# Kernel tuning notes

Hardware: AMD Instinct MI355X
Metric: run time of the kernel (lower is better)

The kernel has to match this reference:

```python
import jax, jax.numpy as jnp
import numpy as np

B, N, C = 512, 252, 256  # N == C - 4 (class axis for torch-style CE over dim 1)


def setup_inputs() -> dict:
    key = jax.random.key(0)
    k1, k2, k3, k4, k5 = jax.random.split(key, 5)
    # output in (0,1): channel 0 feeds BCE (needs open interval), channel 3 gets sqrt'ed
    output = jax.random.uniform(k1, (B, N, C), dtype=jnp.float32) * 0.98 + 0.01
    # target: ch0 presence {0,1}, ch1..3 positive coords, ch4 integer class idx, rest filler
    presence = (jax.random.uniform(k2, (B, N)) < 0.7).astype(jnp.float32)
    coords = jax.random.uniform(k3, (B, N, 3), dtype=jnp.float32) * 0.9 + 0.05
    # per-batch permutation of class ids -> scatter is collision-free & deterministic
    cls = jax.vmap(lambda k: jax.random.permutation(k, N))(jax.random.split(k4, B))
    rest = jax.random.uniform(k5, (B, N, C - 5), dtype=jnp.float32)
    target = jnp.concatenate(
        [presence[:, :, None], coords, cls.astype(jnp.float32)[:, :, None], rest], axis=2
    )
    return {"output": output, "target": target}


def reference(output, target):
    Bb, Nn, Cc = output.shape
    # --- BCE on objectness (mean reduction) ---
    p = output[:, :, 0]
    t = target[:, :, 0]
    bce = -jnp.mean(t * jnp.log(p) + (1.0 - t) * jnp.log1p(-p))

    # --- vectorized masked scatter/reorder (replaces triple python loop) ---
    mask = t != 0  # [B, N]
    cls = target[:, :, 4].astype(jnp.int32)  # class index per box
    filtered = jnp.where(mask[:, :, None], output, 0.0)  # filtered_output
    bidx = jnp.arange(Bb)[:, None]
    idx = jnp.where(mask, cls, Nn)  # route absent boxes to dummy row Nn
    sorted_t = (
        jnp.zeros((Bb, Nn + 1, Cc), output.dtype).at[bidx, idx].set(target)[:, :Nn]
    )

    # --- CE: torch semantics, class axis = dim 1, spatial = dim 2 (size C-4 == N) ---
    tgt_cls = sorted_t[:, :, 4].astype(jnp.int32)  # [B, N] (spatial targets)
    logits = filtered[:, :, 4:]  # [B, N_classes, N_spatial]
    logp = jax.nn.log_softmax(logits, axis=1)
    picked = jnp.take_along_axis(logp, tgt_cls[:, None, :], axis=1)  # [B,1,N]
    ce = -jnp.mean(picked)

    # --- MSE terms ---
    Lx = jnp.mean((filtered[:, :, 1] - sorted_t[:, :, 1]) ** 2)
    Ly = jnp.mean((filtered[:, :, 2] - sorted_t[:, :, 2]) ** 2)
    Lwh = jnp.mean((jnp.sqrt(filtered[:, :, 3]) - jnp.sqrt(sorted_t[:, :, 3])) ** 2)
    mse = Lx + Ly + 2.0 * Lwh

    return 10.0 * mse + bce + 0.5 * (1.0 - bce) + ce
```

## Files before the change

### kernel.cpp

```cpp
#include <hip/hip_runtime.h>
#include <math.h>

#define BB 512
#define NN 252
#define CC 256
#define NW 16

__global__ __launch_bounds__(1024) void detloss_main(const float* __restrict__ outp,
                                                     const float* __restrict__ tgtp,
                                                     float* __restrict__ acc) {
    __shared__ float s_c1[NN], s_c2[NN], s_c3[NN];
    __shared__ float s_diag[NN], s_row0[NN];
    __shared__ float s_part[NW * NN];
    __shared__ float s_red[5];
    __shared__ int s_mask[NN];
    __shared__ int s_fill[NN];
    __shared__ int s_cnt;

    const int b = blockIdx.x;
    const int tid = threadIdx.x;
    const float* ob = outp + (size_t)b * NN * CC;
    const float* tb = tgtp + (size_t)b * NN * CC;

    if (tid < NN) {
        s_c1[tid] = 0.f; s_c2[tid] = 0.f; s_c3[tid] = 0.f;
        s_diag[tid] = 0.f; s_row0[tid] = 0.f; s_fill[tid] = 0;
    }
    if (tid < 5) s_red[tid] = 0.f;
    if (tid == 0) s_cnt = 0;
    __syncthreads();

    float bce_c = 0.f, ce_c = 0.f, lx_c = 0.f, ly_c = 0.f, lwh_c = 0.f;
    float4 o4 = make_float4(0.f, 0.f, 0.f, 0.f);
    bool m = false;

    if (tid < NN) {
        const float4 t4 = *(const float4*)(tb + (size_t)tid * CC);
        const float tcls = tb[(size_t)tid * CC + 4];
        o4 = *(const float4*)(ob + (size_t)tid * CC);
        const float t0 = t4.x;
        bce_c = -(t0 * __logf(o4.x) + (1.f - t0) * log1pf(-o4.x));
        m = (t0 != 0.f);
        s_mask[tid] = m ? 1 : 0;
        if (m) {
            const int j = (int)tcls;
            s_c1[j] = t4.y; s_c2[j] = t4.z; s_c3[j] = t4.w; s_fill[j] = 1;
        } else {
            atomicAdd(&s_cnt, 1);
        }
    }
    __syncthreads();

    if (tid < NN) {
        const float f1 = m ? o4.y : 0.f;
        const float f2 = m ? o4.z : 0.f;
        const float f3 = m ? o4.w : 0.f;
        const float d1 = f1 - s_c1[tid];
        const float d2 = f2 - s_c2[tid];
        const float d3 = sqrtf(f3) - sqrtf(s_c3[tid]);
        lx_c = d1 * d1; ly_c = d2 * d2; lwh_c = d3 * d3;
    }

    const int wave = tid >> 6;
    const int lane = tid & 63;
    if (lane < 63) {
        const float* base = ob + 4 + 4 * lane;
        float4 sum = make_float4(0.f, 0.f, 0.f, 0.f);
        #pragma unroll 4
        for (int n = wave; n < NN; n += NW) {
            if (s_mask[n]) {
                const float4 v = *(const float4*)(base + (size_t)n * CC);
                sum.x += __expf(v.x);
                sum.y += __expf(v.y);
                sum.z += __expf(v.z);
                sum.w += __expf(v.w);
                if ((n >> 2) == lane) {
                    const int r = n & 3;
                    s_diag[n] = (r == 0) ? v.x : (r == 1) ? v.y : (r == 2) ? v.z : v.w;
                }
                if (n == 0) {
                    s_row0[4*lane+0] = v.x; s_row0[4*lane+1] = v.y;
                    s_row0[4*lane+2] = v.z; s_row0[4*lane+3] = v.w;
                }
            }
        }
        const int o = wave * NN + 4 * lane;
        s_part[o+0] = sum.x; s_part[o+1] = sum.y; s_part[o+2] = sum.z; s_part[o+3] = sum.w;
    }
    __syncthreads();

    if (tid < NN) {
        float s = (float)s_cnt;
        #pragma unroll
        for (int w = 0; w < NW; ++w) s += s_part[w * NN + tid];
        const float lse = __logf(s);
        ce_c = lse - (s_fill[tid] ? s_diag[tid] : s_row0[tid]);
    }

    #pragma unroll
    for (int off = 32; off > 0; off >>= 1) {
        bce_c += __shfl_down(bce_c, off);
        ce_c  += __shfl_down(ce_c,  off);
        lx_c  += __shfl_down(lx_c,  off);
        ly_c  += __shfl_down(ly_c,  off);
        lwh_c += __shfl_down(lwh_c, off);
    }
    if (lane == 0) {
        atomicAdd(&s_red[0], bce_c);
        atomicAdd(&s_red[1], ce_c);
        atomicAdd(&s_red[2], lx_c);
        atomicAdd(&s_red[3], ly_c);
        atomicAdd(&s_red[4], lwh_c);
    }
    __syncthreads();
    if (tid < 5) atomicAdd(&acc[tid], s_red[tid]);
}

__global__ void detloss_final(const float* __restrict__ acc, float* __restrict__ outv) {
    const float inv = 1.0f / (float)(BB * NN);
    const float bce = acc[0] * inv;
    const float ce  = acc[1] * inv;
    const float lx  = acc[2] * inv;
    const float ly  = acc[3] * inv;
    const float lwh = acc[4] * inv;
    const float mse = lx + ly + 2.f * lwh;
    outv[0] = 10.f * mse + bce + 0.5f * (1.f - bce) + ce;
}

extern "C" void kernel_launch(void* const* d_in, const int* in_sizes, int n_in,
                              void* d_out, int out_size, void* d_ws, size_t ws_size,
                              hipStream_t stream) {
    const float* outp = (const float*)d_in[0];
    const float* tgtp = (const float*)d_in[1];
    float* acc = (float*)d_ws;
    hipMemsetAsync(acc, 0, 5 * sizeof(float), stream);
    detloss_main<<<BB, 1024, 0, stream>>>(outp, tgtp, acc);
    detloss_final<<<1, 1, 0, stream>>>(acc, (float*)d_out);
}
```

Baseline: 249.1 us.

## Compact masked rows into a list, use nontemporal loads, and drop the memset

Each block now builds a compacted list of present rows in shared memory with an atomic slot counter. The logsumexp loop then runs only over those rows instead of testing a mask on all rows, which removes branch divergence and loop iterations. Logit loads are nontemporal, and the launch bounds request more occupancy. Per-block partial sums go to a workspace array that a 512-thread final kernel reduces, which removes the hipMemsetAsync and the global atomics at the cost of a slightly larger final kernel.

```diff
diff --git a/kernel.cpp b/kernel.cpp
--- a/kernel.cpp
+++ b/kernel.cpp
@@ -6,16 +6,19 @@
 #define CC 256
 #define NW 16
 
-__global__ __launch_bounds__(1024) void detloss_main(const float* __restrict__ outp,
-                                                     const float* __restrict__ tgtp,
-                                                     float* __restrict__ acc) {
+typedef float vf4 __attribute__((ext_vector_type(4)));
+
+
+__global__ __launch_bounds__(1024, 8) void detloss_main(const float* __restrict__ outp,
+                                                        const float* __restrict__ tgtp,
+                                                        float* __restrict__ part) {
     __shared__ float s_c1[NN], s_c2[NN], s_c3[NN];
     __shared__ float s_diag[NN], s_row0[NN];
     __shared__ float s_part[NW * NN];
     __shared__ float s_red[5];
-    __shared__ int s_mask[NN];
+    __shared__ short s_rows[NN];
     __shared__ int s_fill[NN];
-    __shared__ int s_cnt;
+    __shared__ int s_nm;
 
     const int b = blockIdx.x;
     const int tid = threadIdx.x;
@@ -27,7 +30,7 @@
         s_diag[tid] = 0.f; s_row0[tid] = 0.f; s_fill[tid] = 0;
     }
     if (tid < 5) s_red[tid] = 0.f;
-    if (tid == 0) s_cnt = 0;
+    if (tid == 0) s_nm = 0;
     __syncthreads();
 
     float bce_c = 0.f, ce_c = 0.f, lx_c = 0.f, ly_c = 0.f, lwh_c = 0.f;
@@ -41,12 +44,11 @@
         const float t0 = t4.x;
         bce_c = -(t0 * __logf(o4.x) + (1.f - t0) * log1pf(-o4.x));
         m = (t0 != 0.f);
-        s_mask[tid] = m ? 1 : 0;
         if (m) {
             const int j = (int)tcls;
             s_c1[j] = t4.y; s_c2[j] = t4.z; s_c3[j] = t4.w; s_fill[j] = 1;
-        } else {
-            atomicAdd(&s_cnt, 1);
+            const int slot = atomicAdd(&s_nm, 1);
+            s_rows[slot] = (short)tid;
         }
     }
     __syncthreads();
@@ -63,34 +65,33 @@
 
     const int wave = tid >> 6;
     const int lane = tid & 63;
+    const int nm = s_nm;
     if (lane < 63) {
         const float* base = ob + 4 + 4 * lane;
-        float4 sum = make_float4(0.f, 0.f, 0.f, 0.f);
-        #pragma unroll 4
-        for (int n = wave; n < NN; n += NW) {
-            if (s_mask[n]) {
-                const float4 v = *(const float4*)(base + (size_t)n * CC);
-                sum.x += __expf(v.x);
-                sum.y += __expf(v.y);
-                sum.z += __expf(v.z);
-                sum.w += __expf(v.w);
-                if ((n >> 2) == lane) {
-                    const int r = n & 3;
-                    s_diag[n] = (r == 0) ? v.x : (r == 1) ? v.y : (r == 2) ? v.z : v.w;
-                }
-                if (n == 0) {
-                    s_row0[4*lane+0] = v.x; s_row0[4*lane+1] = v.y;
-                    s_row0[4*lane+2] = v.z; s_row0[4*lane+3] = v.w;
-                }
+        float sx = 0.f, sy = 0.f, sz = 0.f, sw = 0.f;
+        for (int i = wave; i < nm; i += NW) {
+            const int n = s_rows[i];
+            const vf4 v = __builtin_nontemporal_load((const vf4*)(base + (size_t)n * CC));
+            sx += __expf(v.x);
+            sy += __expf(v.y);
+            sz += __expf(v.z);
+            sw += __expf(v.w);
+            if ((n >> 2) == lane) {
+                const int r = n & 3;
+                s_diag[n] = (r == 0) ? v.x : (r == 1) ? v.y : (r == 2) ? v.z : v.w;
+            }
+            if (n == 0) {
+                s_row0[4*lane+0] = v.x; s_row0[4*lane+1] = v.y;
+                s_row0[4*lane+2] = v.z; s_row0[4*lane+3] = v.w;
             }
         }
         const int o = wave * NN + 4 * lane;
-        s_part[o+0] = sum.x; s_part[o+1] = sum.y; s_part[o+2] = sum.z; s_part[o+3] = sum.w;
+        s_part[o+0] = sx; s_part[o+1] = sy; s_part[o+2] = sz; s_part[o+3] = sw;
     }
     __syncthreads();
 
     if (tid < NN) {
-        float s = (float)s_cnt;
+        float s = (float)(NN - nm);
         #pragma unroll
         for (int w = 0; w < NW; ++w) s += s_part[w * NN + tid];
         const float lse = __logf(s);
@@ -113,18 +114,48 @@
         atomicAdd(&s_red[4], lwh_c);
     }
     __syncthreads();
-    if (tid < 5) atomicAdd(&acc[tid], s_red[tid]);
+    if (tid < 5) part[tid * BB + b] = s_red[tid];
 }
 
-__global__ void detloss_final(const float* __restrict__ acc, float* __restrict__ outv) {
-    const float inv = 1.0f / (float)(BB * NN);
-    const float bce = acc[0] * inv;
-    const float ce  = acc[1] * inv;
-    const float lx  = acc[2] * inv;
-    const float ly  = acc[3] * inv;
-    const float lwh = acc[4] * inv;
-    const float mse = lx + ly + 2.f * lwh;
-    outv[0] = 10.f * mse + bce + 0.5f * (1.f - bce) + ce;
+__global__ __launch_bounds__(512) void detloss_final(const float* __restrict__ part,
+                                                     float* __restrict__ outv) {
+    __shared__ float s_red[5];
+    const int tid = threadIdx.x;
+    const int lane = tid & 63;
+    if (tid < 5) s_red[tid] = 0.f;
+    __syncthreads();
+
+    float v0 = part[0 * BB + tid];
+    float v1 = part[1 * BB + tid];
+    float v2 = part[2 * BB + tid];
+    float v3 = part[3 * BB + tid];
+    float v4 = part[4 * BB + tid];
+    #pragma unroll
+    for (int off = 32; off > 0; off >>= 1) {
+        v0 += __shfl_down(v0, off);
+        v1 += __shfl_down(v1, off);
+        v2 += __shfl_down(v2, off);
+        v3 += __shfl_down(v3, off);
+        v4 += __shfl_down(v4, off);
+    }
+    if (lane == 0) {
+        atomicAdd(&s_red[0], v0);
+        atomicAdd(&s_red[1], v1);
+        atomicAdd(&s_red[2], v2);
+        atomicAdd(&s_red[3], v3);
+        atomicAdd(&s_red[4], v4);
+    }
+    __syncthreads();
+    if (tid == 0) {
+        const float inv = 1.0f / (float)(BB * NN);
+        const float bce = s_red[0] * inv;
+        const float ce  = s_red[1] * inv;
+        const float lx  = s_red[2] * inv;
+        const float ly  = s_red[3] * inv;
+        const float lwh = s_red[4] * inv;
+        const float mse = lx + ly + 2.f * lwh;
+        outv[0] = 10.f * mse + bce + 0.5f * (1.f - bce) + ce;
+    }
 }
 
 extern "C" void kernel_launch(void* const* d_in, const int* in_sizes, int n_in,
@@ -132,8 +163,7 @@
                               hipStream_t stream) {
     const float* outp = (const float*)d_in[0];
     const float* tgtp = (const float*)d_in[1];
-    float* acc = (float*)d_ws;
-    hipMemsetAsync(acc, 0, 5 * sizeof(float), stream);
-    detloss_main<<<BB, 1024, 0, stream>>>(outp, tgtp, acc);
-    detloss_final<<<1, 1, 0, stream>>>(acc, (float*)d_out);
+    float* part = (float*)d_ws;
+    detloss_main<<<BB, 1024, 0, stream>>>(outp, tgtp, part);
+    detloss_final<<<1, 512, 0, stream>>>(part, (float*)d_out);
 }
```

Measured after the change: 236.5 us (median of 2 runs). 1.05x faster.
